# Performance work log

Hardware: AMD Instinct MI355X
Metric: run time of the kernel (lower is better)

## Reference

```python
import jax, jax.numpy as jnp
import numpy as np
import math

H = 1024
B, S, L = 8, 2048, 1536

def setup_inputs() -> dict:
    key = jax.random.key(0)
    ks = jax.random.split(key, 7)
    hidden_states = jax.random.normal(ks[0], (B, S, H), dtype=jnp.float32)
    advisor_states = jax.random.normal(ks[1], (B, L, H), dtype=jnp.float32)
    advisor_ids = jax.random.randint(ks[2], (B, L), 0, 8, dtype=jnp.int64)
    scale = 1.0 / math.sqrt(H)
    Wq = jax.random.normal(ks[3], (H, H), dtype=jnp.float32) * scale
    Wk = jax.random.normal(ks[4], (H, H), dtype=jnp.float32) * scale
    Wv = jax.random.normal(ks[5], (H, H), dtype=jnp.float32) * scale
    Wo = jax.random.normal(ks[6], (H, H), dtype=jnp.float32) * scale
    return {"hidden_states": hidden_states, "advisor_states": advisor_states,
            "advisor_ids": advisor_ids, "Wq": Wq, "Wk": Wk, "Wv": Wv, "Wo": Wo}

def reference(hidden_states, advisor_states, advisor_ids, Wq, Wk, Wv, Wo):
    b, l, h = advisor_states.shape
    t = l // 3
    # triplet view: [b, t, 3, h]
    trip = advisor_states.reshape(b, t, 3, h)
    ids = advisor_ids.reshape(b, t, 3)
    # value projection on all triplet slots (Linear: x @ W^T)
    vproj = jnp.einsum('btkh,oh->btko', trip, Wv)
    v_rel, v1, v2 = vproj[:, :, 0], vproj[:, :, 1], vproj[:, :, 2]
    rel = ids[:, :, 0][..., None]  # [b, t, 1]
    # vectorized logic-gate value selection over the triplet axis
    is_and = (rel == 0).astype(vproj.dtype)
    is_or = (rel == 1).astype(vproj.dtype)
    is_not = (rel == 2).astype(vproj.dtype)
    is_imp = (rel == 3).astype(vproj.dtype)
    is_xor = (rel == 4).astype(vproj.dtype)
    is_lrn = (rel >= 5).astype(vproj.dtype)
    v_final = (is_and * jnp.minimum(v1, v2)
               + is_or * jnp.maximum(v1, v2)
               + is_not * (-v1)
               + is_imp * jnp.maximum(-v1, v2)
               + is_xor * jnp.abs(v1 - v2)
               + is_lrn * v_rel)  # [b, t, h]
    k_final = jnp.einsum('bth,oh->bto', trip[:, :, 0, :], Wk)
    q = jnp.einsum('bsh,oh->bso', hidden_states, Wq)
    scores = jnp.einsum('bsh,bth->bst', q, k_final) / jnp.sqrt(jnp.float32(h))
    attn = jax.nn.softmax(scores, axis=-1)
    context = jnp.einsum('bst,bth->bsh', attn, v_final)
    return jnp.einsum('bsh,oh->bso', context, Wo)
```

## Files before the change

### kernel.cpp

```cpp
#include <hip/hip_runtime.h>
#include <hip/hip_bf16.h>


typedef unsigned short u16;
typedef __attribute__((ext_vector_type(8))) short bf16x8;
typedef __attribute__((ext_vector_type(4))) float f32x4;
typedef __attribute__((ext_vector_type(4))) unsigned short u16x4;

__device__ __forceinline__ u16 f2bf(float f) {
    __hip_bfloat16 h = __float2bfloat16(f);
    return *reinterpret_cast<u16*>(&h);
}
__device__ __forceinline__ float bf2f(u16 u) {
    __hip_bfloat16 h;
    *reinterpret_cast<u16*>(&h) = u;
    return __bfloat162float(h);
}

__device__ __forceinline__ void gload_lds16(const u16* g, u16* l) {
    __builtin_amdgcn_global_load_lds(
        (const __attribute__((address_space(1))) void*)g,
        (__attribute__((address_space(3))) void*)l, 16, 0, 0);
}

__device__ __forceinline__ void store_c(float* p, float v) { *p = v; }
__device__ __forceinline__ void store_c(u16* p, float v)   { *p = f2bf(v); }

template <int BM, int BN, int WM, int WN, typename TC>
__global__ __launch_bounds__(WM*WN*64, 2) void gemm_pipe(
    const u16* __restrict__ A, const u16* __restrict__ B, TC* __restrict__ C,
    int K, int lda, int ldb, int ldc,
    long sA, long sB, long sC, float alpha,
    int gx, int gy, int q, int r)
{
    constexpr int NT   = WM * WN * 64;
    constexpr int MREP = BM / (WM * 16);
    constexpr int NREP = BN / (WN * 16);
    constexpr int MH   = MREP / 2;
    constexpr int CHA  = BM * 8 / NT;
    constexpr int CHB  = BN * 8 / NT;

    __shared__ u16 As[2][BM * 64];
    __shared__ u16 Bs[2][BN * 64];

    const int orig = blockIdx.x;
    const int xcd  = orig & 7, lo = orig >> 3;
    const int swz  = (xcd < r ? xcd * (q + 1) : r * (q + 1) + (xcd - r) * q) + lo;
    const int bx   = swz % gx;
    const int tmp2 = swz / gx;
    const int by   = tmp2 % gy;
    const int bz   = tmp2 / gy;

    const u16* Ab = A + (long)bz * sA + (long)by * BM * lda;
    const u16* Bb = B + (long)bz * sB + (long)bx * BN * ldb;

    const int tid = threadIdx.x;
    const int l   = tid & 63;
    const int wid = tid >> 6;
    const int wr  = (wid / WN) * (MREP * 16);
    const int wc  = (wid % WN) * (NREP * 16);
    const int lr  = l & 15;
    const int shi = l >> 4;

    auto stage = [&](int buf, int k0) {
#pragma unroll
        for (int i = 0; i < CHA; ++i) {
            const int c = tid + i * NT, row = c >> 3, p = c & 7;
            gload_lds16(Ab + (long)row * lda + k0 + ((p ^ (row & 7)) << 3),
                        &As[buf][c << 3]);
        }
#pragma unroll
        for (int i = 0; i < CHB; ++i) {
            const int c = tid + i * NT, row = c >> 3, p = c & 7;
            gload_lds16(Bb + (long)row * ldb + k0 + ((p ^ (row & 7)) << 3),
                        &Bs[buf][c << 3]);
        }
    };
    auto rdA = [&](int buf, int m, int ks) -> bf16x8 {
        const int row = wr + m * 16 + lr, slot = ks * 4 + shi;
        return *(const bf16x8*)&As[buf][row * 64 + ((slot ^ (row & 7)) << 3)];
    };
    auto rdB = [&](int buf, int n, int ks) -> bf16x8 {
        const int row = wc + n * 16 + lr, slot = ks * 4 + shi;
        return *(const bf16x8*)&Bs[buf][row * 64 + ((slot ^ (row & 7)) << 3)];
    };

    f32x4 acc[MREP][NREP] = {};
    const int nk = K / 64;

    stage(0, 0);
    stage(1, 64);
    asm volatile("s_waitcnt vmcnt(8)" ::: "memory");
    __builtin_amdgcn_sched_barrier(0);
    __builtin_amdgcn_s_barrier();

    int cur = 0;
    for (int t = 0; t < nk; ++t) {
        bf16x8 bfr[NREP][2];
#pragma unroll
        for (int n = 0; n < NREP; ++n) {
            bfr[n][0] = rdB(cur, n, 0);
            bfr[n][1] = rdB(cur, n, 1);
        }
        bf16x8 af[MH][2];
#pragma unroll
        for (int m = 0; m < MH; ++m) {
            af[m][0] = rdA(cur, m, 0);
            af[m][1] = rdA(cur, m, 1);
        }
        __builtin_amdgcn_s_setprio(1);
#pragma unroll
        for (int m = 0; m < MH; ++m)
#pragma unroll
            for (int n = 0; n < NREP; ++n) {
                acc[m][n] = __builtin_amdgcn_mfma_f32_16x16x32_bf16(
                    af[m][0], bfr[n][0], acc[m][n], 0, 0, 0);
                acc[m][n] = __builtin_amdgcn_mfma_f32_16x16x32_bf16(
                    af[m][1], bfr[n][1], acc[m][n], 0, 0, 0);
            }
        __builtin_amdgcn_s_setprio(0);

        bf16x8 ah[MH][2];
#pragma unroll
        for (int m = 0; m < MH; ++m) {
            ah[m][0] = rdA(cur, MH + m, 0);
            ah[m][1] = rdA(cur, MH + m, 1);
        }
        asm volatile("s_waitcnt lgkmcnt(0)" ::: "memory");
        __builtin_amdgcn_sched_barrier(0);
        __builtin_amdgcn_s_barrier();
        if (t + 2 < nk) stage(cur, (t + 2) * 64);
        __builtin_amdgcn_s_setprio(1);
#pragma unroll
        for (int m = 0; m < MH; ++m)
#pragma unroll
            for (int n = 0; n < NREP; ++n) {
                acc[MH + m][n] = __builtin_amdgcn_mfma_f32_16x16x32_bf16(
                    ah[m][0], bfr[n][0], acc[MH + m][n], 0, 0, 0);
                acc[MH + m][n] = __builtin_amdgcn_mfma_f32_16x16x32_bf16(
                    ah[m][1], bfr[n][1], acc[MH + m][n], 0, 0, 0);
            }
        __builtin_amdgcn_s_setprio(0);
        if (t + 2 < nk) {
            asm volatile("s_waitcnt vmcnt(8)" ::: "memory");
        } else {
            asm volatile("s_waitcnt vmcnt(0)" ::: "memory");
        }
        __builtin_amdgcn_sched_barrier(0);
        __builtin_amdgcn_s_barrier();
        cur ^= 1;
    }

    TC*        Cb = C + (long)bz * sC;
    const long rB = (long)by * BM + wr + (l >> 4) * 4;
    const long cB = (long)bx * BN + wc + lr;
#pragma unroll
    for (int m = 0; m < MREP; ++m)
#pragma unroll
        for (int n = 0; n < NREP; ++n)
#pragma unroll
            for (int j = 0; j < 4; ++j)
                store_c(&Cb[(rB + m * 16 + j) * ldc + cB + n * 16],
                        acc[m][n][j] * alpha);
}

template <int BM, int BN, int WM, int WN, typename TC>
static inline void run_gemm(hipStream_t s, const u16* A, const u16* B, TC* C,
                            int M, int N, int K, int lda, int ldb, int ldc,
                            long sA, long sB, long sC, float alpha, int batch)
{
    const int gx = N / BN, gy = M / BM;
    const int nwg = gx * gy * batch;
    gemm_pipe<BM, BN, WM, WN, TC><<<nwg, WM * WN * 64, 0, s>>>(
        A, B, C, K, lda, ldb, ldc, sA, sB, sC, alpha, gx, gy, nwg / 8, nwg % 8);
}

__global__ __launch_bounds__(256) void cvt_f32_bf16(
    const float* __restrict__ in, u16* __restrict__ out, long n)
{
    long i = ((long)blockIdx.x * 256 + threadIdx.x) * 4;
    if (i >= n) return;
    float4 v = *(const float4*)(in + i);
    u16x4 w = { f2bf(v.x), f2bf(v.y), f2bf(v.z), f2bf(v.w) };
    *(u16x4*)(out + i) = w;
}

__global__ __launch_bounds__(256) void cvt_w4(
    const float* __restrict__ w0, const float* __restrict__ w1,
    const float* __restrict__ w2, const float* __restrict__ w3,
    u16* __restrict__ out)
{
    const float* src = (blockIdx.y == 0) ? w0 : (blockIdx.y == 1) ? w1
                     : (blockIdx.y == 2) ? w2 : w3;
    long i = ((long)blockIdx.x * 256 + threadIdx.x) * 4;
    float4 v = *(const float4*)(src + i);
    u16x4 w = { f2bf(v.x), f2bf(v.y), f2bf(v.z), f2bf(v.w) };
    *(u16x4*)(out + (long)blockIdx.y * 1048576 + i) = w;
}

__global__ __launch_bounds__(256) void combine_v(
    const u16* __restrict__ vp, const int* __restrict__ ids,
    u16* __restrict__ Vt)
{
    __shared__ u16 tile[64][68];
    const int b  = blockIdx.z;
    const int t0 = blockIdx.x * 64;
    const int o0 = blockIdx.y * 64;
    const int tx = threadIdx.x;
    const int ty = threadIdx.y;

#pragma unroll
    for (int i = 0; i < 4; ++i) {
        const int  tloc = ty + i * 16;
        const int  t    = t0 + tloc;
        const long base = ((long)(b * 512 + t) * 3) * 1024 + o0 + tx * 4;
        const int  rel  = ids[(b * 512 + t) * 3];
        u16x4 r0 = *(const u16x4*)(vp + base);
        u16x4 r1 = *(const u16x4*)(vp + base + 1024);
        u16x4 r2 = *(const u16x4*)(vp + base + 2048);
#pragma unroll
        for (int c = 0; c < 4; ++c) {
            float vr = bf2f(r0[c]);
            float x1 = bf2f(r1[c]);
            float x2 = bf2f(r2[c]);
            float vf;
            switch (rel) {
                case 0:  vf = fminf(x1, x2);  break;
                case 1:  vf = fmaxf(x1, x2);  break;
                case 2:  vf = -x1;            break;
                case 3:  vf = fmaxf(-x1, x2); break;
                case 4:  vf = fabsf(x1 - x2); break;
                default: vf = vr;             break;
            }
            tile[tloc][tx * 4 + c] = f2bf(vf);
        }
    }
    __syncthreads();
#pragma unroll
    for (int j = 0; j < 4; ++j) {
        const int ol = ty + j * 16;
        u16x4 w;
#pragma unroll
        for (int c = 0; c < 4; ++c) w[c] = tile[tx * 4 + c][ol];
        *(u16x4*)(Vt + ((long)(b * 1024 + o0 + ol)) * 512 + t0 + tx * 4) = w;
    }
}

__global__ __launch_bounds__(256) void softmax_rows(
    const float* __restrict__ S, u16* __restrict__ P)
{
    const int row = blockIdx.x * 4 + (threadIdx.x >> 6);
    const int l   = threadIdx.x & 63;
    const float4* src = (const float4*)(S + (long)row * 512);
    float4 a = src[l];
    float4 b = src[64 + l];

    float m = fmaxf(fmaxf(fmaxf(a.x, a.y), fmaxf(a.z, a.w)),
                    fmaxf(fmaxf(b.x, b.y), fmaxf(b.z, b.w)));
#pragma unroll
    for (int off = 32; off; off >>= 1) m = fmaxf(m, __shfl_xor(m, off));

    a.x = __expf(a.x - m); a.y = __expf(a.y - m);
    a.z = __expf(a.z - m); a.w = __expf(a.w - m);
    b.x = __expf(b.x - m); b.y = __expf(b.y - m);
    b.z = __expf(b.z - m); b.w = __expf(b.w - m);

    float s = a.x + a.y + a.z + a.w + b.x + b.y + b.z + b.w;
#pragma unroll
    for (int off = 32; off; off >>= 1) s += __shfl_xor(s, off);
    const float inv = 1.0f / s;

    u16x4 w0 = { f2bf(a.x * inv), f2bf(a.y * inv), f2bf(a.z * inv), f2bf(a.w * inv) };
    u16x4 w1 = { f2bf(b.x * inv), f2bf(b.y * inv), f2bf(b.z * inv), f2bf(b.w * inv) };
    u16x4* dst = (u16x4*)(P + (long)row * 512);
    dst[l]      = w0;
    dst[64 + l] = w1;
}

extern "C" void kernel_launch(void* const* d_in, const int* in_sizes, int n_in,
                              void* d_out, int out_size, void* d_ws, size_t ws_size,
                              hipStream_t stream)
{
    const float* hidden  = (const float*)d_in[0];
    const float* advisor = (const float*)d_in[1];
    const int*   ids     = (const int*)d_in[2];
    const float* Wq      = (const float*)d_in[3];
    const float* Wk      = (const float*)d_in[4];
    const float* Wv      = (const float*)d_in[5];
    const float* Wo      = (const float*)d_in[6];
    float*       out     = (float*)d_out;

    char* ws = (char*)d_ws;
    const long MB = 1L << 20;
    u16*   Wq_bf  = (u16*)(ws + 0 * MB);
    u16*   Hbf    = (u16*)(ws + 8 * MB);
    float* scores = (float*)(ws + 8 * MB);
    u16*   Abf    = (u16*)(ws + 40 * MB);
    u16*   P      = (u16*)(ws + 40 * MB);
    u16*   Qbf    = (u16*)(ws + 64 * MB);
    u16*   ctx    = (u16*)(ws + 64 * MB);
    u16*   Kf     = (u16*)(ws + 96 * MB);
    u16*   Vt     = (u16*)(ws + 104 * MB);
    u16*   vp     = (u16*)(ws + 112 * MB);

    u16* Wk_bf = Wq_bf + 1048576;
    u16* Wv_bf = Wq_bf + 2097152;
    u16* Wo_bf = Wq_bf + 3145728;

    cvt_f32_bf16<<<16384, 256, 0, stream>>>(hidden,  Hbf, 16777216L);
    cvt_f32_bf16<<<12288, 256, 0, stream>>>(advisor, Abf, 12582912L);
    cvt_w4<<<dim3(1024, 4), 256, 0, stream>>>(Wq, Wk, Wv, Wo, Wq_bf);

    run_gemm<256, 256, 2, 4, u16>(stream, Hbf, Wq_bf, Qbf,
        16384, 1024, 1024, 1024, 1024, 1024, 0, 0, 0, 1.0f, 1);
    run_gemm<128, 128, 2, 2, u16>(stream, Abf, Wk_bf, Kf,
        4096, 1024, 1024, 3072, 1024, 1024, 0, 0, 0, 1.0f, 1);
    run_gemm<256, 256, 2, 4, u16>(stream, Abf, Wv_bf, vp,
        12288, 1024, 1024, 1024, 1024, 1024, 0, 0, 0, 1.0f, 1);

    combine_v<<<dim3(8, 16, 8), dim3(16, 16), 0, stream>>>(vp, ids, Vt);

    run_gemm<128, 128, 2, 2, float>(stream, Qbf, Kf, scores,
        2048, 512, 1024, 1024, 1024, 512,
        2048L * 1024, 512L * 1024, 2048L * 512, 0.03125f, 8);

    softmax_rows<<<4096, 256, 0, stream>>>(scores, P);

    run_gemm<128, 128, 2, 2, u16>(stream, P, Vt, ctx,
        2048, 1024, 512, 512, 512, 1024,
        2048L * 512, 1024L * 512, 2048L * 1024, 1.0f, 8);

    run_gemm<256, 256, 2, 4, float>(stream, ctx, Wo_bf, out,
        16384, 1024, 1024, 1024, 1024, 1024, 0, 0, 0, 1.0f, 1);
}
```

Before: 361.1 us.

## Add 8-wave four-phase pipelined 256x256 GEMM for large projections

Adds a new 512-thread GEMM kernel that splits each K-step into four MFMA phases, interleaving LDS fragment reads and prefetches of the next-next K tile between phases, with barriers and raised wave priority around MFMA blocks. It also uses XCD-aware block swizzling. The Q, V and output projections switch to this kernel to overlap global loads, LDS reads and matrix math better than the prior 256-thread pipeline. The cost is more threads per block, more barriers and higher register pressure, which may limit occupancy.

```diff
diff --git a/kernel.cpp b/kernel.cpp
--- a/kernel.cpp
+++ b/kernel.cpp
@@ -25,6 +25,161 @@
 
 __device__ __forceinline__ void store_c(float* p, float v) { *p = v; }
 __device__ __forceinline__ void store_c(u16* p, float v)   { *p = f2bf(v); }
+
+template <typename TC>
+__global__ __launch_bounds__(512, 2) void gemm_8ph(
+    const u16* __restrict__ A, const u16* __restrict__ B, TC* __restrict__ C,
+    int K, int lda, int ldb, int ldc, float alpha, int gx, int q, int r)
+{
+    __shared__ u16 As[2][256 * 64];
+    __shared__ u16 Bs[2][256 * 64];
+
+    const int orig = blockIdx.x;
+    const int xcd  = orig & 7, lo = orig >> 3;
+    const int swz  = (xcd < r ? xcd * (q + 1) : r * (q + 1) + (xcd - r) * q) + lo;
+    const int bx   = swz % gx;
+    const int by   = swz / gx;
+
+    const u16* Ab = A + (long)by * 256 * lda;
+    const u16* Bb = B + (long)bx * 256 * ldb;
+
+    const int tid = threadIdx.x;
+    const int l   = tid & 63;
+    const int wid = tid >> 6;
+    const int wr  = (wid >> 2) * 128;
+    const int wc  = (wid & 3) * 64;
+    const int lr  = l & 15;
+    const int shi = l >> 4;
+
+    auto stageA = [&](int buf, int k0) {
+#pragma unroll
+        for (int i = 0; i < 4; ++i) {
+            const int c = tid + i * 512, row = c >> 3, p = c & 7;
+            gload_lds16(Ab + (long)row * lda + k0 + ((p ^ (row & 7)) << 3),
+                        &As[buf][c << 3]);
+        }
+    };
+    auto stageB = [&](int buf, int k0) {
+#pragma unroll
+        for (int i = 0; i < 4; ++i) {
+            const int c = tid + i * 512, row = c >> 3, p = c & 7;
+            gload_lds16(Bb + (long)row * ldb + k0 + ((p ^ (row & 7)) << 3),
+                        &Bs[buf][c << 3]);
+        }
+    };
+    auto rdA = [&](int buf, int m, int ks) -> bf16x8 {
+        const int row = wr + m * 16 + lr, slot = ks * 4 + shi;
+        return *(const bf16x8*)&As[buf][row * 64 + ((slot ^ (row & 7)) << 3)];
+    };
+    auto rdB = [&](int buf, int n, int ks) -> bf16x8 {
+        const int row = wc + n * 16 + lr, slot = ks * 4 + shi;
+        return *(const bf16x8*)&Bs[buf][row * 64 + ((slot ^ (row & 7)) << 3)];
+    };
+
+    f32x4 acc[8][4] = {};
+    const int nk = K / 64;
+
+    stageA(0, 0);  stageB(0, 0);
+    stageA(1, 64); stageB(1, 64);
+    asm volatile("s_waitcnt vmcnt(8)" ::: "memory");
+    __builtin_amdgcn_sched_barrier(0);
+    __builtin_amdgcn_s_barrier();
+
+    for (int t = 0; t < nk; ++t) {
+        const int  cur  = t & 1;
+        const bool pre  = (t + 2 < nk);
+        const int  k2   = (t + 2) * 64;
+        bf16x8 af[4][2], bl[2][2], bh[2][2];
+
+#pragma unroll
+        for (int m = 0; m < 4; ++m) { af[m][0] = rdA(cur, m, 0); af[m][1] = rdA(cur, m, 1); }
+#pragma unroll
+        for (int n = 0; n < 2; ++n) { bl[n][0] = rdB(cur, n, 0); bl[n][1] = rdB(cur, n, 1); }
+        __builtin_amdgcn_s_barrier();
+        asm volatile("s_waitcnt lgkmcnt(0)" ::: "memory");
+        __builtin_amdgcn_sched_barrier(0);
+        __builtin_amdgcn_s_setprio(1);
+#pragma unroll
+        for (int m = 0; m < 4; ++m)
+#pragma unroll
+            for (int n = 0; n < 2; ++n) {
+                acc[m][n] = __builtin_amdgcn_mfma_f32_16x16x32_bf16(af[m][0], bl[n][0], acc[m][n], 0, 0, 0);
+                acc[m][n] = __builtin_amdgcn_mfma_f32_16x16x32_bf16(af[m][1], bl[n][1], acc[m][n], 0, 0, 0);
+            }
+        __builtin_amdgcn_s_setprio(0);
+        __builtin_amdgcn_s_barrier();
+
+#pragma unroll
+        for (int n = 0; n < 2; ++n) { bh[n][0] = rdB(cur, 2 + n, 0); bh[n][1] = rdB(cur, 2 + n, 1); }
+        __builtin_amdgcn_s_barrier();
+        asm volatile("s_waitcnt lgkmcnt(0)" ::: "memory");
+        __builtin_amdgcn_sched_barrier(0);
+        __builtin_amdgcn_s_setprio(1);
+#pragma unroll
+        for (int m = 0; m < 4; ++m)
+#pragma unroll
+            for (int n = 0; n < 2; ++n) {
+                acc[m][2 + n] = __builtin_amdgcn_mfma_f32_16x16x32_bf16(af[m][0], bh[n][0], acc[m][2 + n], 0, 0, 0);
+                acc[m][2 + n] = __builtin_amdgcn_mfma_f32_16x16x32_bf16(af[m][1], bh[n][1], acc[m][2 + n], 0, 0, 0);
+            }
+        __builtin_amdgcn_s_setprio(0);
+        __builtin_amdgcn_s_barrier();
+
+#pragma unroll
+        for (int m = 0; m < 4; ++m) { af[m][0] = rdA(cur, 4 + m, 0); af[m][1] = rdA(cur, 4 + m, 1); }
+        if (pre) stageB(cur, k2);
+        __builtin_amdgcn_s_barrier();
+        asm volatile("s_waitcnt lgkmcnt(0)" ::: "memory");
+        __builtin_amdgcn_sched_barrier(0);
+        __builtin_amdgcn_s_setprio(1);
+#pragma unroll
+        for (int m = 0; m < 4; ++m)
+#pragma unroll
+            for (int n = 0; n < 2; ++n) {
+                acc[4 + m][2 + n] = __builtin_amdgcn_mfma_f32_16x16x32_bf16(af[m][0], bh[n][0], acc[4 + m][2 + n], 0, 0, 0);
+                acc[4 + m][2 + n] = __builtin_amdgcn_mfma_f32_16x16x32_bf16(af[m][1], bh[n][1], acc[4 + m][2 + n], 0, 0, 0);
+            }
+        __builtin_amdgcn_s_setprio(0);
+        __builtin_amdgcn_s_barrier();
+
+        if (pre) stageA(cur, k2);
+        __builtin_amdgcn_s_barrier();
+        __builtin_amdgcn_s_setprio(1);
+#pragma unroll
+        for (int m = 0; m < 4; ++m)
+#pragma unroll
+            for (int n = 0; n < 2; ++n) {
+                acc[4 + m][n] = __builtin_amdgcn_mfma_f32_16x16x32_bf16(af[m][0], bl[n][0], acc[4 + m][n], 0, 0, 0);
+                acc[4 + m][n] = __builtin_amdgcn_mfma_f32_16x16x32_bf16(af[m][1], bl[n][1], acc[4 + m][n], 0, 0, 0);
+            }
+        __builtin_amdgcn_s_setprio(0);
+        if (pre) { asm volatile("s_waitcnt vmcnt(8)" ::: "memory"); }
+        else     { asm volatile("s_waitcnt vmcnt(0)" ::: "memory"); }
+        __builtin_amdgcn_sched_barrier(0);
+        __builtin_amdgcn_s_barrier();
+    }
+
+    const long rB = (long)by * 256 + wr + (l >> 4) * 4;
+    const long cB = (long)bx * 256 + wc + lr;
+#pragma unroll
+    for (int m = 0; m < 8; ++m)
+#pragma unroll
+        for (int n = 0; n < 4; ++n)
+#pragma unroll
+            for (int j = 0; j < 4; ++j)
+                store_c(&C[(rB + m * 16 + j) * ldc + cB + n * 16],
+                        acc[m][n][j] * alpha);
+}
+
+template <typename TC>
+static inline void run_gemm8(hipStream_t s, const u16* A, const u16* B, TC* C,
+                             int M, int N, int K, int lda, int ldb, int ldc,
+                             float alpha)
+{
+    const int gx = N / 256, nwg = gx * (M / 256);
+    gemm_8ph<TC><<<nwg, 512, 0, s>>>(A, B, C, K, lda, ldb, ldc, alpha,
+                                     gx, nwg / 8, nwg % 8);
+}
 
 template <int BM, int BN, int WM, int WN, typename TC>
 __global__ __launch_bounds__(WM*WN*64, 2) void gemm_pipe(
@@ -311,12 +466,12 @@
     cvt_f32_bf16<<<12288, 256, 0, stream>>>(advisor, Abf, 12582912L);
     cvt_w4<<<dim3(1024, 4), 256, 0, stream>>>(Wq, Wk, Wv, Wo, Wq_bf);
 
-    run_gemm<256, 256, 2, 4, u16>(stream, Hbf, Wq_bf, Qbf,
-        16384, 1024, 1024, 1024, 1024, 1024, 0, 0, 0, 1.0f, 1);
+    run_gemm8<u16>(stream, Hbf, Wq_bf, Qbf, 16384, 1024, 1024,
+                   1024, 1024, 1024, 1.0f);
     run_gemm<128, 128, 2, 2, u16>(stream, Abf, Wk_bf, Kf,
         4096, 1024, 1024, 3072, 1024, 1024, 0, 0, 0, 1.0f, 1);
-    run_gemm<256, 256, 2, 4, u16>(stream, Abf, Wv_bf, vp,
-        12288, 1024, 1024, 1024, 1024, 1024, 0, 0, 0, 1.0f, 1);
+    run_gemm8<u16>(stream, Abf, Wv_bf, vp, 12288, 1024, 1024,
+                   1024, 1024, 1024, 1.0f);
 
     combine_v<<<dim3(8, 16, 8), dim3(16, 16), 0, stream>>>(vp, ids, Vt);
 
@@ -330,6 +485,6 @@
         2048, 1024, 512, 512, 512, 1024,
         2048L * 512, 1024L * 512, 2048L * 1024, 1.0f, 8);
 
-    run_gemm<256, 256, 2, 4, float>(stream, ctx, Wo_bf, out,
-        16384, 1024, 1024, 1024, 1024, 1024, 0, 0, 0, 1.0f, 1);
-}
+    run_gemm8<float>(stream, ctx, Wo_bf, out, 16384, 1024, 1024,
+                     1024, 1024, 1024, 1.0f);
+}
```

New measurement: 367.2 us. No clear change (+1.7%).
